# Kernel optimization log

Hardware: AMD Instinct MI355X
Metric: run time of the kernel (lower is better)

The kernel has to match this reference:

```python
import jax, jax.numpy as jnp
import numpy as np

B, S, D = 32, 4096, 256


def setup_inputs() -> dict:
    key = jax.random.key(0)
    kx, km = jax.random.split(key)
    x = jax.random.normal(kx, (B, S, D), dtype=jnp.float32)
    # keep_mask[b, t] == 1 means timestep t is kept (original: 1 - bernoulli(skipping_probs))
    keep_mask = jax.random.randint(km, (B, S), 0, 2, dtype=jnp.int32)
    return {"x": x, "keep_mask": keep_mask}


def reference(x, keep_mask):
    # Batched stream-compaction: move kept timesteps to the front of each row
    # (stable, preserving original order), zero-pad the tail.
    keep = keep_mask.astype(bool)                       # [B, S]
    # stable argsort of (not keep): kept indices first, in original time order
    order = jnp.argsort(jnp.logical_not(keep), axis=1, stable=True)  # [B, S]
    gathered = jnp.take_along_axis(x, order[:, :, None], axis=1)      # [B, S, D]
    counts = jnp.sum(keep, axis=1, keepdims=True)       # [B, 1] kept lengths
    valid = jnp.arange(S)[None, :] < counts             # [B, S]
    return gathered * valid[:, :, None].astype(x.dtype)
```

## Files before the change

kernel.cpp:

```cpp
#include <hip/hip_runtime.h>

constexpr int S_LEN = 4096;
constexpr int D_DIM = 256;
constexpr int ROWS_PER_BLOCK = 16;
constexpr int BLOCK_THREADS  = ROWS_PER_BLOCK * 64;
constexpr int BLOCKS_PER_BATCH = S_LEN / ROWS_PER_BLOCK;

__global__ __launch_bounds__(BLOCK_THREADS)
void fused_compact_kernel(const float* __restrict__ x,
                          const int* __restrict__ mask,
                          float* __restrict__ out) {
    const int b   = blockIdx.x / BLOCKS_PER_BATCH;
    const int blk = blockIdx.x % BLOCKS_PER_BATCH;
    const int t0  = blk * ROWS_PER_BLOCK;

    __shared__ int wtot[16];
    __shared__ int spos[ROWS_PER_BLOCK];
    __shared__ int skeep[ROWS_PER_BLOCK];

    const int tid  = threadIdx.x;
    const int lane = tid & 63;
    const int wid  = tid >> 6;

    const int e0 = tid * 4;
    int4 m = *reinterpret_cast<const int4*>(mask + b * S_LEN + e0);
    int v[4] = {m.x, m.y, m.z, m.w};
    const int tot = v[0] + v[1] + v[2] + v[3];

    int scan = tot;
#pragma unroll
    for (int off = 1; off < 64; off <<= 1) {
        int n = __shfl_up(scan, off, 64);
        if (lane >= off) scan += n;
    }
    if (lane == 63) wtot[wid] = scan;
    __syncthreads();

    int wexcl = 0, cnt = 0;
#pragma unroll
    for (int i = 0; i < 16; ++i) {
        int w = wtot[i];
        if (i < wid) wexcl += w;
        cnt += w;
    }

    int excl = wexcl + (scan - tot);

#pragma unroll
    for (int i = 0; i < 4; ++i) {
        int r = (e0 + i) - t0;
        if ((unsigned)r < (unsigned)ROWS_PER_BLOCK) {
            spos[r]  = excl;
            skeep[r] = v[i];
        }
        excl += v[i];
    }
    __syncthreads();

    const int t    = t0 + wid;
    const int keep = skeep[wid];
    const int p    = spos[wid];
    const int orow = keep ? p : (cnt + (t - p));

    const size_t in_off  = ((size_t)b * S_LEN + t)    * D_DIM;
    const size_t out_off = ((size_t)b * S_LEN + orow) * D_DIM;

    float4 val = make_float4(0.f, 0.f, 0.f, 0.f);
    if (keep) val = reinterpret_cast<const float4*>(x + in_off)[lane];
    reinterpret_cast<float4*>(out + out_off)[lane] = val;
}

extern "C" void kernel_launch(void* const* d_in, const int* in_sizes, int n_in,
                              void* d_out, int out_size, void* d_ws, size_t ws_size,
                              hipStream_t stream) {
    const float* x    = (const float*)d_in[0];
    const int*   mask = (const int*)d_in[1];
    float*       out  = (float*)d_out;

    const int B = in_sizes[1] / S_LEN;
    const int grid = B * BLOCKS_PER_BATCH;

    fused_compact_kernel<<<grid, BLOCK_THREADS, 0, stream>>>(x, mask, out);
}
```

Before: 232.3 us.

## Split into one-pass per-batch scan kernel and sync-free scatter kernel

Replaces the fused kernel, where every block re-scanned the full mask row of its batch, with a two-kernel scheme. A per-batch scan kernel computes each timestep's destination row once and stores it bit-encoded (negated for dropped rows) in workspace. A scatter kernel then reads one index per row and copies or zeroes it without shared memory or barriers. This removes the redundant scanning and synchronisation, at the cost of an extra launch and a workspace round trip.

Result: faster. 221.7 us, median of 2 (-4.6%).

```diff
diff --git a/kernel.cpp b/kernel.cpp
--- a/kernel.cpp
+++ b/kernel.cpp
@@ -2,28 +2,18 @@
 
 constexpr int S_LEN = 4096;
 constexpr int D_DIM = 256;
-constexpr int ROWS_PER_BLOCK = 16;
-constexpr int BLOCK_THREADS  = ROWS_PER_BLOCK * 64;
-constexpr int BLOCKS_PER_BATCH = S_LEN / ROWS_PER_BLOCK;
 
-__global__ __launch_bounds__(BLOCK_THREADS)
-void fused_compact_kernel(const float* __restrict__ x,
-                          const int* __restrict__ mask,
-                          float* __restrict__ out) {
-    const int b   = blockIdx.x / BLOCKS_PER_BATCH;
-    const int blk = blockIdx.x % BLOCKS_PER_BATCH;
-    const int t0  = blk * ROWS_PER_BLOCK;
-
-    __shared__ int wtot[16];
-    __shared__ int spos[ROWS_PER_BLOCK];
-    __shared__ int skeep[ROWS_PER_BLOCK];
-
-    const int tid  = threadIdx.x;
+__global__ __launch_bounds__(1024)
+void scan_kernel(const int* __restrict__ mask,
+                 int* __restrict__ orow_enc) {
+    const int b   = blockIdx.x;
+    const int tid = threadIdx.x;
     const int lane = tid & 63;
     const int wid  = tid >> 6;
+    __shared__ int wtot[16];
 
-    const int e0 = tid * 4;
-    int4 m = *reinterpret_cast<const int4*>(mask + b * S_LEN + e0);
+    const int base = b * S_LEN + tid * 4;
+    int4 m = *reinterpret_cast<const int4*>(mask + base);
     int v[4] = {m.x, m.y, m.z, m.w};
     const int tot = v[0] + v[1] + v[2] + v[3];
 
@@ -46,21 +36,27 @@
 
     int excl = wexcl + (scan - tot);
 
-#pragma unroll
-    for (int i = 0; i < 4; ++i) {
-        int r = (e0 + i) - t0;
-        if ((unsigned)r < (unsigned)ROWS_PER_BLOCK) {
-            spos[r]  = excl;
-            skeep[r] = v[i];
-        }
-        excl += v[i];
-    }
-    __syncthreads();
+    int4 e;
+    int t = tid * 4;
+    e.x = v[0] ? excl : ~(cnt + (t + 0 - excl)); excl += v[0];
+    e.y = v[1] ? excl : ~(cnt + (t + 1 - excl)); excl += v[1];
+    e.z = v[2] ? excl : ~(cnt + (t + 2 - excl)); excl += v[2];
+    e.w = v[3] ? excl : ~(cnt + (t + 3 - excl));
+    *reinterpret_cast<int4*>(orow_enc + base) = e;
+}
 
-    const int t    = t0 + wid;
-    const int keep = skeep[wid];
-    const int p    = spos[wid];
-    const int orow = keep ? p : (cnt + (t - p));
+__global__ __launch_bounds__(512)
+void scatter_kernel(const float* __restrict__ x,
+                    const int* __restrict__ orow_enc,
+                    float* __restrict__ out) {
+    const int lane = threadIdx.x & 63;
+    const int w    = blockIdx.x * 8 + (threadIdx.x >> 6);
+    const int b = w >> 12;
+    const int t = w & (S_LEN - 1);
+
+    const int e    = orow_enc[w];
+    const bool keep = (e >= 0);
+    const int orow  = keep ? e : ~e;
 
     const size_t in_off  = ((size_t)b * S_LEN + t)    * D_DIM;
     const size_t out_off = ((size_t)b * S_LEN + orow) * D_DIM;
@@ -78,7 +74,11 @@
     float*       out  = (float*)d_out;
 
     const int B = in_sizes[1] / S_LEN;
-    const int grid = B * BLOCKS_PER_BATCH;
 
-    fused_compact_kernel<<<grid, BLOCK_THREADS, 0, stream>>>(x, mask, out);
+    int* orow_enc = (int*)d_ws;
+
+    scan_kernel<<<B, 1024, 0, stream>>>(mask, orow_enc);
+
+    const int rows = B * S_LEN;
+    scatter_kernel<<<rows / 8, 512, 0, stream>>>(x, orow_enc, out);
 }
```
